# Kernel tuning notes

Measured on AMD Instinct MI355X. Metric: run time of the kernel, lower is better.

Reference implementation:

```python
import jax, jax.numpy as jnp
import numpy as np

N_RAYS = 131072
N_SAMPLES = 64
N_IMPORTANCE = 128
NEAR, FAR = 2.0, 6.0


def setup_inputs() -> dict:
    key = jax.random.key(0)
    k1, k2, k3, k4 = jax.random.split(key, 4)
    rays_o = jax.random.normal(k1, (N_RAYS, 3), dtype=jnp.float32)
    rays_d = jax.random.normal(k2, (N_RAYS, 3), dtype=jnp.float32)
    # z_vals must be monotonically increasing per ray (bin edges from coarse sampler)
    z_vals = jnp.sort(
        jax.random.uniform(k3, (N_RAYS, N_SAMPLES), dtype=jnp.float32,
                           minval=NEAR, maxval=FAR), axis=-1)
    weights = jax.random.uniform(k4, (N_RAYS, N_SAMPLES), dtype=jnp.float32)
    return {"rays_o": rays_o, "rays_d": rays_d, "z_vals": z_vals, "weights": weights}


def _sample_pdf(bins, weights):
    # bins: [N, B], weights: [N, B-1]; det=True since perturb == 0.0
    w = weights + 1e-5
    pdf = w / jnp.sum(w, axis=-1, keepdims=True)
    cdf = jnp.cumsum(pdf, axis=-1)
    cdf = jnp.concatenate([jnp.zeros_like(cdf[..., :1]), cdf], axis=-1)  # [N, B]
    u = jnp.linspace(0.0, 1.0, N_IMPORTANCE, dtype=cdf.dtype)
    u = jnp.broadcast_to(u, cdf.shape[:-1] + (N_IMPORTANCE,))  # [N, NI]
    # per-ray binary search (right=True)
    inds = jax.vmap(lambda c, uu: jnp.searchsorted(c, uu, side='right'))(cdf, u)
    below = jnp.maximum(inds - 1, 0)
    above = jnp.minimum(inds, cdf.shape[-1] - 1)
    cdf_b = jnp.take_along_axis(cdf, below, axis=-1)
    cdf_a = jnp.take_along_axis(cdf, above, axis=-1)
    bins_b = jnp.take_along_axis(bins, below, axis=-1)
    bins_a = jnp.take_along_axis(bins, above, axis=-1)
    denom = cdf_a - cdf_b
    denom = jnp.where(denom < 1e-5, jnp.ones_like(denom), denom)
    t = (u - cdf_b) / denom
    return bins_b + t * (bins_a - bins_b)  # [N, NI]


def reference(rays_o, rays_d, z_vals, weights):
    z_mid = 0.5 * (z_vals[..., 1:] + z_vals[..., :-1])          # [N, S-1]
    z_samples = _sample_pdf(z_mid, weights[..., 1:-1])           # [N, NI]
    z_samples = jax.lax.stop_gradient(z_samples)                 # .detach()
    z_all = jnp.sort(jnp.concatenate([z_vals, z_samples], -1), -1)  # [N, S+NI]
    pts = rays_o[:, None, :] + rays_d[:, None, :] * z_all[..., None]  # [N, S+NI, 3]
    return pts, z_all, z_samples
```

## Files before the change

kernel.cpp:

```cpp
#include <hip/hip_runtime.h>

#define NRAYS 131072
#define NS 64
#define NI 128
#define NM 63
#define NW 62
#define NT 192

__global__ __launch_bounds__(256) void importance_kernel(
    const float* __restrict__ rays_o,
    const float* __restrict__ rays_d,
    const float* __restrict__ z_vals,
    const float* __restrict__ weights,
    float* __restrict__ out_pts,
    float* __restrict__ out_zall,
    float* __restrict__ out_zs)
{
    __shared__ float s_zall[4][NT];

    const int wave = threadIdx.x >> 6;
    const int lane = threadIdx.x & 63;
    const int ray  = (blockIdx.x << 2) + wave;

    const float* zv_g = z_vals  + (size_t)ray * NS;
    const float* w_g  = weights + (size_t)ray * NS;

    const float zvl = zv_g[lane];
    float od = 0.0f;
    if (lane < 6)
        od = (lane < 3) ? rays_o[ray * 3 + lane] : rays_d[ray * 3 + lane - 3];
    const float wl = (lane < NW) ? (w_g[lane + 1] + 1e-5f) : 0.0f;

    const float o0 = __shfl(od, 0, 64), o1 = __shfl(od, 1, 64), o2 = __shfl(od, 2, 64);
    const float d0 = __shfl(od, 3, 64), d1 = __shfl(od, 4, 64), d2 = __shfl(od, 5, 64);

    const float zm = 0.5f * (zvl + __shfl_down(zvl, 1, 64));

    float scan = wl;
    #pragma unroll
    for (int off = 1; off < 64; off <<= 1) {
        const float up = __shfl_up(scan, off, 64);
        if (lane >= off) scan += up;
    }
    const float total = __shfl(scan, NW - 1, 64);
    const float sp  = __shfl_up(scan, 1, 64);
    const float cdf = (lane == 0) ? 0.0f : sp / total;

    float xv[2]; int xb[2];
    #pragma unroll
    for (int rep = 0; rep < 2; rep++) {
        const int j = lane + (rep << 6);
        const float u = (float)((double)j * (1.0 / 127.0));
        int lo = 0, hi = NM;
        #pragma unroll
        for (int it = 0; it < 6; it++) {
            const int mid = (lo + hi) >> 1;
            const float v = __shfl(cdf, mid, 64);
            if (lo < hi) { if (v <= u) lo = mid + 1; else hi = mid; }
        }
        int below = lo - 1; if (below < 0) below = 0;
        int above = lo;     if (above > NM - 1) above = NM - 1;
        const float cb = __shfl(cdf, below, 64);
        const float ca = __shfl(cdf, above, 64);
        const float bb = __shfl(zm,  below, 64);
        const float ba = __shfl(zm,  above, 64);
        float denom = ca - cb;
        if (denom < 1e-5f) denom = 1.0f;
        const float t = (u - cb) / denom;
        xv[rep] = bb + t * (ba - bb);
        xb[rep] = below;
    }
    const float zs0 = xv[0], zs1 = xv[1];

    {
        int lo = 0, hi = NI;
        #pragma unroll
        for (int it = 0; it < 8; it++) {
            const int mid = (lo + hi) >> 1;
            const int m6  = mid & 63;
            const float v0 = __shfl(zs0, m6, 64);
            const float v1 = __shfl(zs1, m6, 64);
            const float v  = (mid < 64) ? v0 : v1;
            if (lo < hi) { if (v < zvl) lo = mid + 1; else hi = mid; }
        }
        s_zall[wave][lane + lo] = zvl;
    }

    #pragma unroll
    for (int rep = 0; rep < 2; rep++) {
        const float x = xv[rep];
        int c = xb[rep] + 1;
        while (true) {
            const int  idx = (c < NS) ? c : (NS - 1);
            const float zc = __shfl(zvl, idx, 64);
            const bool adv = (c < NS) && (zc <= x);
            if (!__any(adv)) break;
            if (adv) c++;
        }
        s_zall[wave][lane + (rep << 6) + c] = x;
    }

    asm volatile("s_waitcnt lgkmcnt(0)" ::: "memory");

    const float* zallp = s_zall[wave];
    const size_t pts_base = (size_t)ray * (NT * 3);
    #pragma unroll
    for (int rep = 0; rep < 9; rep++) {
        const int i = lane + (rep << 6);
        const int k = i / 3;
        const int d = i - 3 * k;
        const float z  = zallp[k];
        const float o  = (d == 0) ? o0 : ((d == 1) ? o1 : o2);
        const float dd = (d == 0) ? d0 : ((d == 1) ? d1 : d2);
        out_pts[pts_base + i] = o + dd * z;
    }
    const size_t za_base = (size_t)ray * NT;
    #pragma unroll
    for (int rep = 0; rep < 3; rep++) {
        const int i = lane + (rep << 6);
        out_zall[za_base + i] = zallp[i];
    }
    const size_t zs_base = (size_t)ray * NI;
    out_zs[zs_base + lane]      = zs0;
    out_zs[zs_base + 64 + lane] = zs1;
}

extern "C" void kernel_launch(void* const* d_in, const int* in_sizes, int n_in,
                              void* d_out, int out_size, void* d_ws, size_t ws_size,
                              hipStream_t stream) {
    const float* rays_o  = (const float*)d_in[0];
    const float* rays_d  = (const float*)d_in[1];
    const float* z_vals  = (const float*)d_in[2];
    const float* weights = (const float*)d_in[3];

    float* out      = (float*)d_out;
    float* out_pts  = out;
    float* out_zall = out + (size_t)NRAYS * NT * 3;
    float* out_zs   = out_zall + (size_t)NRAYS * NT;

    dim3 grid(NRAYS / 4), block(256);
    hipLaunchKernelGGL(importance_kernel, grid, block, 0, stream,
                       rays_o, rays_d, z_vals, weights,
                       out_pts, out_zall, out_zs);
}
```

Measured before the change: 511.1 us.

## Replace merge-position searches with analytic rank via inverse CDF and vectorize stores

Computes each z_val's rank among the importance samples analytically by mapping z_val back through the piecewise-linear CDF to a u value and counting linspace points below it, instead of an 8-step shuffle binary search. The samples' merge positions now come from the known bin index plus one comparison, which drops the data-dependent while-loop with __any. Output stores are widened to float4/float2, and ray origin/direction become scalar loads through readfirstlane. The exact inverse-CDF rank can disagree with the float reference near ties or degenerate bins, which would leave the sort order wrong or leave holes in shared memory.

After: 515.2 us. Within noise of the previous version (+0.8%).

```diff
diff --git a/kernel.cpp b/kernel.cpp
--- a/kernel.cpp
+++ b/kernel.cpp
@@ -16,7 +16,7 @@
     float* __restrict__ out_zall,
     float* __restrict__ out_zs)
 {
-    __shared__ float s_zall[4][NT];
+    __shared__ __align__(16) float s_zall[4][NT];
 
     const int wave = threadIdx.x >> 6;
     const int lane = threadIdx.x & 63;
@@ -26,13 +26,11 @@
     const float* w_g  = weights + (size_t)ray * NS;
 
     const float zvl = zv_g[lane];
-    float od = 0.0f;
-    if (lane < 6)
-        od = (lane < 3) ? rays_o[ray * 3 + lane] : rays_d[ray * 3 + lane - 3];
-    const float wl = (lane < NW) ? (w_g[lane + 1] + 1e-5f) : 0.0f;
+    const float wl  = (lane < NW) ? (w_g[lane + 1] + 1e-5f) : 0.0f;
 
-    const float o0 = __shfl(od, 0, 64), o1 = __shfl(od, 1, 64), o2 = __shfl(od, 2, 64);
-    const float d0 = __shfl(od, 3, 64), d1 = __shfl(od, 4, 64), d2 = __shfl(od, 5, 64);
+    const int sray = __builtin_amdgcn_readfirstlane(ray);
+    const float o0 = rays_o[3 * sray + 0], o1 = rays_o[3 * sray + 1], o2 = rays_o[3 * sray + 2];
+    const float d0 = rays_d[3 * sray + 0], d1 = rays_d[3 * sray + 1], d2 = rays_d[3 * sray + 2];
 
     const float zm = 0.5f * (zvl + __shfl_down(zvl, 1, 64));
 
@@ -46,10 +44,43 @@
     const float sp  = __shfl_up(scan, 1, 64);
     const float cdf = (lane == 0) ? 0.0f : sp / total;
 
-    float xv[2]; int xb[2];
+    const float zm_m1  = __shfl_up(zm, 1, 64);
+    const float cdf_m1 = __shfl_up(cdf, 1, 64);
+
+    float U;
+    {
+        float rr = (zvl - zm_m1) / (zm - zm_m1);
+        rr = fminf(fmaxf(rr, 0.0f), 1.0f);
+        float dg = cdf - cdf_m1;
+        if (dg < 1e-5f) dg = 1.0f;
+        float uu = cdf_m1 + rr * dg;
+        uu = fminf(uu, cdf);
+        U = (lane == 0) ? 0.0f : ((lane == 63) ? 2.0f : uu);
+    }
+
+    int cnt;
+    if (lane == 0) cnt = 0;
+    else if (lane == 63) cnt = 128;
+    else {
+        const int g = (int)(U * 127.0f);
+        int c = g - 1;
+        #pragma unroll
+        for (int t = -1; t <= 1; ++t) {
+            const int j = g + t;
+            bool lt;
+            if (j < 0) lt = true;
+            else if (j > 127) lt = false;
+            else lt = ((float)((double)j * (1.0 / 127.0)) < U);
+            c += lt ? 1 : 0;
+        }
+        cnt = c;
+    }
+    s_zall[wave][lane + cnt] = zvl;
+
+    float xs0, xs1;
     #pragma unroll
     for (int rep = 0; rep < 2; rep++) {
-        const int j = lane + (rep << 6);
+        const int j = (lane << 1) + rep;
         const float u = (float)((double)j * (1.0 / 127.0));
         int lo = 0, hi = NM;
         #pragma unroll
@@ -58,71 +89,59 @@
             const float v = __shfl(cdf, mid, 64);
             if (lo < hi) { if (v <= u) lo = mid + 1; else hi = mid; }
         }
-        int below = lo - 1; if (below < 0) below = 0;
-        int above = lo;     if (above > NM - 1) above = NM - 1;
+        const int below = lo - 1;
+        const int above = (lo > NM - 1) ? (NM - 1) : lo;
         const float cb = __shfl(cdf, below, 64);
         const float ca = __shfl(cdf, above, 64);
         const float bb = __shfl(zm,  below, 64);
         const float ba = __shfl(zm,  above, 64);
+        const float Ul = __shfl(U,   lo,    64);
         float denom = ca - cb;
         if (denom < 1e-5f) denom = 1.0f;
         const float t = (u - cb) / denom;
-        xv[rep] = bb + t * (ba - bb);
-        xb[rep] = below;
-    }
-    const float zs0 = xv[0], zs1 = xv[1];
-
-    {
-        int lo = 0, hi = NI;
-        #pragma unroll
-        for (int it = 0; it < 8; it++) {
-            const int mid = (lo + hi) >> 1;
-            const int m6  = mid & 63;
-            const float v0 = __shfl(zs0, m6, 64);
-            const float v1 = __shfl(zs1, m6, 64);
-            const float v  = (mid < 64) ? v0 : v1;
-            if (lo < hi) { if (v < zvl) lo = mid + 1; else hi = mid; }
-        }
-        s_zall[wave][lane + lo] = zvl;
-    }
-
-    #pragma unroll
-    for (int rep = 0; rep < 2; rep++) {
-        const float x = xv[rep];
-        int c = xb[rep] + 1;
-        while (true) {
-            const int  idx = (c < NS) ? c : (NS - 1);
-            const float zc = __shfl(zvl, idx, 64);
-            const bool adv = (c < NS) && (zc <= x);
-            if (!__any(adv)) break;
-            if (adv) c++;
-        }
-        s_zall[wave][lane + (rep << 6) + c] = x;
+        const float x = bb + t * (ba - bb);
+        const int pos = j + lo + ((Ul <= u) ? 1 : 0);
+        s_zall[wave][pos] = x;
+        if (rep == 0) xs0 = x; else xs1 = x;
     }
 
     asm volatile("s_waitcnt lgkmcnt(0)" ::: "memory");
 
     const float* zallp = s_zall[wave];
+
     const size_t pts_base = (size_t)ray * (NT * 3);
     #pragma unroll
-    for (int rep = 0; rep < 9; rep++) {
-        const int i = lane + (rep << 6);
-        const int k = i / 3;
-        const int d = i - 3 * k;
-        const float z  = zallp[k];
-        const float o  = (d == 0) ? o0 : ((d == 1) ? o1 : o2);
-        const float dd = (d == 0) ? d0 : ((d == 1) ? d1 : d2);
-        out_pts[pts_base + i] = o + dd * z;
+    for (int rep = 0; rep < 3; rep++) {
+        const int i4 = lane + (rep << 6);
+        if (i4 < 144) {
+            const int q  = i4 / 3;
+            const int m  = i4 - 3 * q;
+            const int k0 = i4 + q;
+            const float za = zallp[k0];
+            const float zb = zallp[k0 + 1];
+            float4 v;
+            #pragma unroll
+            for (int t = 0; t < 4; t++) {
+                const int mt = m + t;
+                const float z  = (mt >= 3) ? zb : za;
+                const int  ds  = (mt >= 3) ? (mt - 3) : mt;
+                const float oo = (ds == 0) ? o0 : ((ds == 1) ? o1 : o2);
+                const float dd = (ds == 0) ? d0 : ((ds == 1) ? d1 : d2);
+                (&v.x)[t] = fmaf(dd, z, oo);
+            }
+            *reinterpret_cast<float4*>(out_pts + pts_base + ((size_t)i4 << 2)) = v;
+        }
     }
-    const size_t za_base = (size_t)ray * NT;
-    #pragma unroll
-    for (int rep = 0; rep < 3; rep++) {
-        const int i = lane + (rep << 6);
-        out_zall[za_base + i] = zallp[i];
+
+    if (lane < 48) {
+        const float4 v = *reinterpret_cast<const float4*>(&zallp[lane << 2]);
+        *reinterpret_cast<float4*>(out_zall + (size_t)ray * NT + (lane << 2)) = v;
     }
-    const size_t zs_base = (size_t)ray * NI;
-    out_zs[zs_base + lane]      = zs0;
-    out_zs[zs_base + 64 + lane] = zs1;
+
+    {
+        float2 zz; zz.x = xs0; zz.y = xs1;
+        *reinterpret_cast<float2*>(out_zs + (size_t)ray * NI + (lane << 1)) = zz;
+    }
 }
 
 extern "C" void kernel_launch(void* const* d_in, const int* in_sizes, int n_in,
```
